# Optimization experiments

Hardware: AMD Instinct MI355X
Metric: run time of the kernel (lower is better)

The kernel has to match this reference:

```python
import jax, jax.numpy as jnp
import numpy as np
import math

B, SQ, SK, D = 16, 2048, 2048, 64


def setup_inputs() -> dict:
    key = jax.random.key(0)
    kq, kk, kv, kl = jax.random.split(key, 4)
    queries = jax.random.normal(kq, (B, SQ, D), dtype=jnp.float32)
    keys = jax.random.normal(kk, (B, SK, D), dtype=jnp.float32)
    values = jax.random.normal(kv, (B, SK, D), dtype=jnp.float32)
    # valid key lengths in [1, SK]
    valid_lens = jax.random.randint(kl, (B,), 1, SK + 1, dtype=jnp.int32)
    return {"queries": queries, "keys": keys, "values": values, "valid_lens": valid_lens}


def reference(queries, keys, values, valid_lens):
    d = queries.shape[-1]
    # [B, SQ, SK] raw scores
    scores = jnp.einsum("bqd,bkd->bqk", queries, keys) / math.sqrt(d)
    # masked_softmax: key positions >= valid_len are set to -1e6 (d2l semantics)
    kpos = jnp.arange(scores.shape[-1], dtype=jnp.int32)  # [SK]
    mask = kpos[None, None, :] < valid_lens[:, None, None]  # [B,1,SK] -> broadcast
    scores = jnp.where(mask, scores, jnp.float32(-1e6))
    attn = jax.nn.softmax(scores, axis=-1)
    # dropout rate is 0.0 -> identity
    return jnp.einsum("bqk,bkd->bqd", attn, values)
```

## Files before the change

### kernel.cpp

```cpp
#include <hip/hip_runtime.h>

#define NB 16
#define SQL 2048
#define SKL 2048
#define DH 64

typedef __attribute__((ext_vector_type(8)))  short bf16x8;
typedef __attribute__((ext_vector_type(4)))  unsigned short u16x4;
typedef __attribute__((ext_vector_type(8)))  unsigned short u16x8;
typedef __attribute__((ext_vector_type(4)))  float f32x4;
typedef __attribute__((ext_vector_type(16))) float f32x16;
typedef __attribute__((ext_vector_type(2)))  unsigned int u32x2;
typedef __attribute__((ext_vector_type(4)))  unsigned int u32x4;

#define SCL 0.18033688011112042f

__device__ __forceinline__ unsigned short f2bf(float f) {
    unsigned int u = __builtin_bit_cast(unsigned int, f);
    u += 0x7fffu + ((u >> 16) & 1u);
    return (unsigned short)(u >> 16);
}
__device__ __forceinline__ float bf2f(unsigned short h) {
    return __builtin_bit_cast(float, (unsigned int)h << 16);
}

__device__ __forceinline__ float fast_exp2(float x) {
#if __has_builtin(__builtin_amdgcn_exp2f)
    return __builtin_amdgcn_exp2f(x);
#else
    return exp2f(x);
#endif
}

__device__ __forceinline__ unsigned int cvt_pk_bf16(float a, float b) {
    unsigned int r;
    asm("v_cvt_pk_bf16_f32 %0, %1, %2" : "=v"(r) : "v"(a), "v"(b));
    return r;
}

__device__ __forceinline__ void lane32_swap(unsigned int &x, unsigned int &y) {
#if __has_builtin(__builtin_amdgcn_permlane32_swap)
    u32x2 r = __builtin_amdgcn_permlane32_swap(x, y, false, false);
    x = r[0]; y = r[1];
#else
    asm volatile("s_nop 1\n\tv_permlane32_swap_b32 %0, %1\n\ts_nop 1"
                 : "+v"(x), "+v"(y));
#endif
}

__global__ __launch_bounds__(256) void prep_kernel(
    const float* __restrict__ V, unsigned short* __restrict__ Vt) {
    const int blk = blockIdx.x;
    const int b   = blk >> 5;
    const int kb  = (blk & 31) << 6;
    __shared__ float tile[64][65];
    const int tid = threadIdx.x;
    {
        const int r  = tid >> 2;
        const int cg = (tid & 3) << 4;
        const float* vsrc = V + ((size_t)b * SKL + (kb + r)) * DH;
        #pragma unroll
        for (int i = 0; i < 4; ++i) {
            float4 x = *(const float4*)(vsrc + cg + i * 4);
            tile[r][cg + i*4 + 0] = x.x;
            tile[r][cg + i*4 + 1] = x.y;
            tile[r][cg + i*4 + 2] = x.z;
            tile[r][cg + i*4 + 3] = x.w;
        }
    }
    __syncthreads();
    {
        const int d  = tid >> 2;
        const int kg = (tid & 3) << 4;
        unsigned short* dst = Vt + ((size_t)b * DH + d) * SKL + kb + kg;
        u16x8 o0, o1;
        #pragma unroll
        for (int j = 0; j < 8; ++j) o0[j] = f2bf(tile[kg + j][d]);
        #pragma unroll
        for (int j = 0; j < 8; ++j) o1[j] = f2bf(tile[kg + 8 + j][d]);
        *(u16x8*)(dst)     = o0;
        *(u16x8*)(dst + 8) = o1;
    }
}

__global__ __launch_bounds__(256, 2) void attn_kernel(
    const float* __restrict__ Qf,
    const float* __restrict__ Kf,
    const unsigned short* __restrict__ Vt,
    const int* __restrict__ valid_lens,
    float* __restrict__ out) {
    const int b    = blockIdx.x;
    const int qblk = blockIdx.y;

    const int valid  = valid_lens[b];
    const int ntiles = (valid + 63) >> 6;

    const int tid  = threadIdx.x;
    const int lane = tid & 63;
    const int l31  = lane & 31;
    const int h2   = lane >> 5;
    const int sw   = l31 & 7;

    __shared__ unsigned short Klds[2][64][64];
    __shared__ unsigned short Vlds[2][64][64];

    const int q0 = qblk * 128 + (tid >> 6) * 32;
    const float* qptr = Qf + ((size_t)b * SQL + q0 + l31) * DH + h2 * 8;
    bf16x8 qf[4];
    #pragma unroll
    for (int ks = 0; ks < 4; ++ks) {
        float4 a0 = *(const float4*)(qptr + ks * 16);
        float4 a1 = *(const float4*)(qptr + ks * 16 + 4);
        u32x4 w = { cvt_pk_bf16(a0.x * SCL, a0.y * SCL),
                    cvt_pk_bf16(a0.z * SCL, a0.w * SCL),
                    cvt_pk_bf16(a1.x * SCL, a1.y * SCL),
                    cvt_pk_bf16(a1.z * SCL, a1.w * SCL) };
        qf[ks] = __builtin_bit_cast(bf16x8, w);
    }

    const float* kbase = Kf + (size_t)b * SKL * DH;
    const unsigned short* vbase = Vt + (size_t)b * DH * SKL;

    f32x16 o[2];
    #pragma unroll
    for (int i = 0; i < 2; ++i)
        #pragma unroll
        for (int r = 0; r < 16; ++r) o[i][r] = 0.f;
    float lr[4] = {0.f, 0.f, 0.f, 0.f};

    float4 kreg[2][2];
    u16x8  vreg[2];
    auto load_tile = [&](int kb0) {
        #pragma unroll
        for (int i = 0; i < 2; ++i) {
            const int c = i * 256 + tid, r = c >> 3, col = (c & 7) << 3;
            const float* kp = kbase + (size_t)(kb0 + r) * DH + col;
            kreg[i][0] = *(const float4*)(kp);
            kreg[i][1] = *(const float4*)(kp + 4);
            vreg[i]    = *(const u16x8*)(vbase + (size_t)r * SKL + kb0 + col);
        }
    };
    auto store_tile = [&](int buf) {
        #pragma unroll
        for (int i = 0; i < 2; ++i) {
            const int c = i * 256 + tid, r = c >> 3;
            const int pc = ((c & 7) ^ (r & 7)) << 3;
            u32x4 w = { cvt_pk_bf16(kreg[i][0].x, kreg[i][0].y),
                        cvt_pk_bf16(kreg[i][0].z, kreg[i][0].w),
                        cvt_pk_bf16(kreg[i][1].x, kreg[i][1].y),
                        cvt_pk_bf16(kreg[i][1].z, kreg[i][1].w) };
            *(u16x8*)&Klds[buf][r][pc] = __builtin_bit_cast(u16x8, w);
            *(u16x8*)&Vlds[buf][r][pc] = vreg[i];
        }
    };

    load_tile(0);
    store_tile(0);
    if (ntiles > 1) load_tile(64);
    __syncthreads();

    for (int kt = 0; kt < ntiles; ++kt) {
        const int kb  = kt << 6;
        const int cur = kt & 1;

        if (kt + 1 < ntiles) {
            store_tile(cur ^ 1);
            if (kt + 2 < ntiles) load_tile(kb + 128);
        }

        f32x16 s[2];
        #pragma unroll
        for (int t = 0; t < 2; ++t)
            #pragma unroll
            for (int r = 0; r < 16; ++r) s[t][r] = 0.f;
        __builtin_amdgcn_s_setprio(1);
        #pragma unroll
        for (int t = 0; t < 2; ++t)
            #pragma unroll
            for (int ks = 0; ks < 4; ++ks) {
                const bf16x8 kf = *(const bf16x8*)
                    &Klds[cur][t * 32 + l31][((2 * ks + h2) ^ sw) << 3];
                s[t] = __builtin_amdgcn_mfma_f32_32x32x16_bf16(kf, qf[ks], s[t], 0, 0, 0);
            }
        __builtin_amdgcn_s_setprio(0);

        if (kb + 64 > valid) {
            #pragma unroll
            for (int t = 0; t < 2; ++t)
                #pragma unroll
                for (int r = 0; r < 16; ++r)
                    if (kb + t * 32 + (r & 3) + 8 * (r >> 2) + 4 * h2 >= valid)
                        s[t][r] = -1e30f;
        }

        #pragma unroll
        for (int t = 0; t < 2; ++t)
            #pragma unroll
            for (int r = 0; r < 16; ++r) {
                const float p = fast_exp2(s[t][r]);
                s[t][r] = p;
                lr[r & 3] += p;
            }

        bf16x8 pf[4];
        #pragma unroll
        for (int t = 0; t < 2; ++t) {
            unsigned int w[4][2];
            #pragma unroll
            for (int a = 0; a < 4; ++a) {
                w[a][0] = cvt_pk_bf16(s[t][4 * a + 0], s[t][4 * a + 1]);
                w[a][1] = cvt_pk_bf16(s[t][4 * a + 2], s[t][4 * a + 3]);
            }
            #pragma unroll
            for (int i = 0; i < 2; ++i) {
                lane32_swap(w[0][i], w[1][i]);
                lane32_swap(w[2][i], w[3][i]);
            }
            u32x4 lo4 = { w[0][0], w[0][1], w[1][0], w[1][1] };
            u32x4 hi4 = { w[2][0], w[2][1], w[3][0], w[3][1] };
            pf[2 * t + 0] = __builtin_bit_cast(bf16x8, lo4);
            pf[2 * t + 1] = __builtin_bit_cast(bf16x8, hi4);
        }

        __builtin_amdgcn_s_setprio(1);
        #pragma unroll
        for (int dt = 0; dt < 2; ++dt)
            #pragma unroll
            for (int ks = 0; ks < 4; ++ks) {
                const bf16x8 vf = *(const bf16x8*)
                    &Vlds[cur][dt * 32 + l31][((2 * ks + h2) ^ sw) << 3];
                o[dt] = __builtin_amdgcn_mfma_f32_32x32x16_bf16(vf, pf[ks], o[dt], 0, 0, 0);
            }
        __builtin_amdgcn_s_setprio(0);

        __syncthreads();
    }

    float lrow = (lr[0] + lr[1]) + (lr[2] + lr[3]);
    lrow += __shfl_xor(lrow, 32);
    const float inv = 1.0f / lrow;

    float* op = out + ((size_t)b * SQL + q0 + l31) * DH;
    #pragma unroll
    for (int dt = 0; dt < 2; ++dt)
        #pragma unroll
        for (int g = 0; g < 4; ++g) {
            f32x4 ow;
            ow[0] = o[dt][g * 4 + 0] * inv; ow[1] = o[dt][g * 4 + 1] * inv;
            ow[2] = o[dt][g * 4 + 2] * inv; ow[3] = o[dt][g * 4 + 3] * inv;
            *(f32x4*)(op + dt * 32 + 8 * g + 4 * h2) = ow;
        }
}

extern "C" void kernel_launch(void* const* d_in, const int* in_sizes, int n_in,
                              void* d_out, int out_size, void* d_ws, size_t ws_size,
                              hipStream_t stream) {
    const float* Q  = (const float*)d_in[0];
    const float* K  = (const float*)d_in[1];
    const float* V  = (const float*)d_in[2];
    const int*   vl = (const int*)d_in[3];
    float* out = (float*)d_out;

    unsigned short* Vt = (unsigned short*)d_ws;

    prep_kernel<<<dim3(512), dim3(256), 0, stream>>>(V, Vt);
    attn_kernel<<<dim3(NB, SQL / 128), dim3(256), 0, stream>>>(
        Q, K, Vt, vl, out);
}
```

Baseline: 102.5 us.

## Split key tiles across wave pairs and merge partial outputs via LDS

Each block now handles 64 queries instead of 128, with 4 waves forming two pairs that process alternating key tiles (a split-K within the block). Partial outputs and row sums from the second pair are reduced through shared memory before the final normalization. This doubles the grid size and halves per-block serial key-loop length, improving parallelism and load balance across batches with varying valid lengths. The cost is doubled K/V global loads per query, more LDS (two tiles per stage), and an extra reduction and sync at the end.

```diff
diff --git a/kernel.cpp b/kernel.cpp
--- a/kernel.cpp
+++ b/kernel.cpp
@@ -19,9 +19,6 @@
     unsigned int u = __builtin_bit_cast(unsigned int, f);
     u += 0x7fffu + ((u >> 16) & 1u);
     return (unsigned short)(u >> 16);
-}
-__device__ __forceinline__ float bf2f(unsigned short h) {
-    return __builtin_bit_cast(float, (unsigned int)h << 16);
 }
 
 __device__ __forceinline__ float fast_exp2(float x) {
@@ -94,17 +91,21 @@
 
     const int valid  = valid_lens[b];
     const int ntiles = (valid + 63) >> 6;
+    const int rounds = (ntiles + 1) >> 1;
 
     const int tid  = threadIdx.x;
+    const int wave = tid >> 6;
+    const int pr   = wave >> 1;
+    const int qg   = wave & 1;
     const int lane = tid & 63;
     const int l31  = lane & 31;
     const int h2   = lane >> 5;
     const int sw   = l31 & 7;
 
-    __shared__ unsigned short Klds[2][64][64];
-    __shared__ unsigned short Vlds[2][64][64];
-
-    const int q0 = qblk * 128 + (tid >> 6) * 32;
+    __shared__ unsigned short Klds[2][2][64][64];
+    __shared__ unsigned short Vlds[2][2][64][64];
+
+    const int q0 = qblk * 64 + qg * 32;
     const float* qptr = Qf + ((size_t)b * SQL + q0 + l31) * DH + h2 * 8;
     bf16x8 qf[4];
     #pragma unroll
@@ -128,128 +129,166 @@
         for (int r = 0; r < 16; ++r) o[i][r] = 0.f;
     float lr[4] = {0.f, 0.f, 0.f, 0.f};
 
-    float4 kreg[2][2];
-    u16x8  vreg[2];
-    auto load_tile = [&](int kb0) {
-        #pragma unroll
-        for (int i = 0; i < 2; ++i) {
-            const int c = i * 256 + tid, r = c >> 3, col = (c & 7) << 3;
-            const float* kp = kbase + (size_t)(kb0 + r) * DH + col;
-            kreg[i][0] = *(const float4*)(kp);
-            kreg[i][1] = *(const float4*)(kp + 4);
-            vreg[i]    = *(const u16x8*)(vbase + (size_t)r * SKL + kb0 + col);
+    float4 kreg[2][2][2];
+    u16x8  vreg[2][2];
+    auto load_round = [&](int R) {
+        #pragma unroll
+        for (int p = 0; p < 2; ++p) {
+            const int ti = 2 * R + p;
+            if (ti < ntiles) {
+                const int kb0 = ti << 6;
+                #pragma unroll
+                for (int i = 0; i < 2; ++i) {
+                    const int c = i * 256 + tid, r = c >> 3, col = (c & 7) << 3;
+                    const float* kp = kbase + (size_t)(kb0 + r) * DH + col;
+                    kreg[p][i][0] = *(const float4*)(kp);
+                    kreg[p][i][1] = *(const float4*)(kp + 4);
+                    vreg[p][i]    = *(const u16x8*)(vbase + (size_t)r * SKL + kb0 + col);
+                }
+            }
         }
     };
-    auto store_tile = [&](int buf) {
-        #pragma unroll
-        for (int i = 0; i < 2; ++i) {
-            const int c = i * 256 + tid, r = c >> 3;
-            const int pc = ((c & 7) ^ (r & 7)) << 3;
-            u32x4 w = { cvt_pk_bf16(kreg[i][0].x, kreg[i][0].y),
-                        cvt_pk_bf16(kreg[i][0].z, kreg[i][0].w),
-                        cvt_pk_bf16(kreg[i][1].x, kreg[i][1].y),
-                        cvt_pk_bf16(kreg[i][1].z, kreg[i][1].w) };
-            *(u16x8*)&Klds[buf][r][pc] = __builtin_bit_cast(u16x8, w);
-            *(u16x8*)&Vlds[buf][r][pc] = vreg[i];
+    auto store_round = [&](int set, int R) {
+        #pragma unroll
+        for (int p = 0; p < 2; ++p) {
+            const int ti = 2 * R + p;
+            if (ti < ntiles) {
+                #pragma unroll
+                for (int i = 0; i < 2; ++i) {
+                    const int c = i * 256 + tid, r = c >> 3;
+                    const int pc = ((c & 7) ^ (r & 7)) << 3;
+                    u32x4 w = { cvt_pk_bf16(kreg[p][i][0].x, kreg[p][i][0].y),
+                                cvt_pk_bf16(kreg[p][i][0].z, kreg[p][i][0].w),
+                                cvt_pk_bf16(kreg[p][i][1].x, kreg[p][i][1].y),
+                                cvt_pk_bf16(kreg[p][i][1].z, kreg[p][i][1].w) };
+                    *(u16x8*)&Klds[set][p][r][pc] = __builtin_bit_cast(u16x8, w);
+                    *(u16x8*)&Vlds[set][p][r][pc] = vreg[p][i];
+                }
+            }
         }
     };
 
-    load_tile(0);
-    store_tile(0);
-    if (ntiles > 1) load_tile(64);
+    load_round(0);
+    store_round(0, 0);
+    if (rounds > 1) load_round(1);
     __syncthreads();
 
-    for (int kt = 0; kt < ntiles; ++kt) {
-        const int kb  = kt << 6;
-        const int cur = kt & 1;
-
-        if (kt + 1 < ntiles) {
-            store_tile(cur ^ 1);
-            if (kt + 2 < ntiles) load_tile(kb + 128);
-        }
-
-        f32x16 s[2];
-        #pragma unroll
-        for (int t = 0; t < 2; ++t)
-            #pragma unroll
-            for (int r = 0; r < 16; ++r) s[t][r] = 0.f;
-        __builtin_amdgcn_s_setprio(1);
-        #pragma unroll
-        for (int t = 0; t < 2; ++t)
-            #pragma unroll
-            for (int ks = 0; ks < 4; ++ks) {
-                const bf16x8 kf = *(const bf16x8*)
-                    &Klds[cur][t * 32 + l31][((2 * ks + h2) ^ sw) << 3];
-                s[t] = __builtin_amdgcn_mfma_f32_32x32x16_bf16(kf, qf[ks], s[t], 0, 0, 0);
-            }
-        __builtin_amdgcn_s_setprio(0);
-
-        if (kb + 64 > valid) {
+    for (int r = 0; r < rounds; ++r) {
+        const int rp = r & 1;
+        if (r + 1 < rounds) {
+            store_round(rp ^ 1, r + 1);
+            if (r + 2 < rounds) load_round(r + 2);
+        }
+
+        const int ti = 2 * r + pr;
+        if (ti < ntiles) {
+            const int kb = ti << 6;
+
+            f32x16 s[2];
             #pragma unroll
             for (int t = 0; t < 2; ++t)
                 #pragma unroll
-                for (int r = 0; r < 16; ++r)
-                    if (kb + t * 32 + (r & 3) + 8 * (r >> 2) + 4 * h2 >= valid)
-                        s[t][r] = -1e30f;
-        }
-
-        #pragma unroll
-        for (int t = 0; t < 2; ++t)
-            #pragma unroll
-            for (int r = 0; r < 16; ++r) {
-                const float p = fast_exp2(s[t][r]);
-                s[t][r] = p;
-                lr[r & 3] += p;
-            }
-
-        bf16x8 pf[4];
-        #pragma unroll
-        for (int t = 0; t < 2; ++t) {
-            unsigned int w[4][2];
-            #pragma unroll
-            for (int a = 0; a < 4; ++a) {
-                w[a][0] = cvt_pk_bf16(s[t][4 * a + 0], s[t][4 * a + 1]);
-                w[a][1] = cvt_pk_bf16(s[t][4 * a + 2], s[t][4 * a + 3]);
-            }
-            #pragma unroll
-            for (int i = 0; i < 2; ++i) {
-                lane32_swap(w[0][i], w[1][i]);
-                lane32_swap(w[2][i], w[3][i]);
-            }
-            u32x4 lo4 = { w[0][0], w[0][1], w[1][0], w[1][1] };
-            u32x4 hi4 = { w[2][0], w[2][1], w[3][0], w[3][1] };
-            pf[2 * t + 0] = __builtin_bit_cast(bf16x8, lo4);
-            pf[2 * t + 1] = __builtin_bit_cast(bf16x8, hi4);
-        }
-
-        __builtin_amdgcn_s_setprio(1);
+                for (int r2 = 0; r2 < 16; ++r2) s[t][r2] = 0.f;
+            __builtin_amdgcn_s_setprio(1);
+            #pragma unroll
+            for (int t = 0; t < 2; ++t)
+                #pragma unroll
+                for (int ks = 0; ks < 4; ++ks) {
+                    const bf16x8 kf = *(const bf16x8*)
+                        &Klds[rp][pr][t * 32 + l31][((2 * ks + h2) ^ sw) << 3];
+                    s[t] = __builtin_amdgcn_mfma_f32_32x32x16_bf16(kf, qf[ks], s[t], 0, 0, 0);
+                }
+            __builtin_amdgcn_s_setprio(0);
+
+            if (kb + 64 > valid) {
+                #pragma unroll
+                for (int t = 0; t < 2; ++t)
+                    #pragma unroll
+                    for (int r2 = 0; r2 < 16; ++r2)
+                        if (kb + t * 32 + (r2 & 3) + 8 * (r2 >> 2) + 4 * h2 >= valid)
+                            s[t][r2] = -1e30f;
+            }
+
+            #pragma unroll
+            for (int t = 0; t < 2; ++t)
+                #pragma unroll
+                for (int r2 = 0; r2 < 16; ++r2) {
+                    const float p = fast_exp2(s[t][r2]);
+                    s[t][r2] = p;
+                    lr[r2 & 3] += p;
+                }
+
+            bf16x8 pf[4];
+            #pragma unroll
+            for (int t = 0; t < 2; ++t) {
+                unsigned int w[4][2];
+                #pragma unroll
+                for (int a = 0; a < 4; ++a) {
+                    w[a][0] = cvt_pk_bf16(s[t][4 * a + 0], s[t][4 * a + 1]);
+                    w[a][1] = cvt_pk_bf16(s[t][4 * a + 2], s[t][4 * a + 3]);
+                }
+                #pragma unroll
+                for (int i = 0; i < 2; ++i) {
+                    lane32_swap(w[0][i], w[1][i]);
+                    lane32_swap(w[2][i], w[3][i]);
+                }
+                u32x4 lo4 = { w[0][0], w[0][1], w[1][0], w[1][1] };
+                u32x4 hi4 = { w[2][0], w[2][1], w[3][0], w[3][1] };
+                pf[2 * t + 0] = __builtin_bit_cast(bf16x8, lo4);
+                pf[2 * t + 1] = __builtin_bit_cast(bf16x8, hi4);
+            }
+
+            __builtin_amdgcn_s_setprio(1);
+            #pragma unroll
+            for (int dt = 0; dt < 2; ++dt)
+                #pragma unroll
+                for (int ks = 0; ks < 4; ++ks) {
+                    const bf16x8 vf = *(const bf16x8*)
+                        &Vlds[rp][pr][dt * 32 + l31][((2 * ks + h2) ^ sw) << 3];
+                    o[dt] = __builtin_amdgcn_mfma_f32_32x32x16_bf16(vf, pf[ks], o[dt], 0, 0, 0);
+                }
+            __builtin_amdgcn_s_setprio(0);
+        }
+
+        __syncthreads();
+    }
+
+    float lrow = (lr[0] + lr[1]) + (lr[2] + lr[3]);
+    float* obuf = (float*)&Klds[0][0][0][0];
+    float* lbuf = obuf + 2 * 32 * 68;
+    if (pr == 1) {
+        const int base = (qg * 32 + l31) * 68;
         #pragma unroll
         for (int dt = 0; dt < 2; ++dt)
             #pragma unroll
-            for (int ks = 0; ks < 4; ++ks) {
-                const bf16x8 vf = *(const bf16x8*)
-                    &Vlds[cur][dt * 32 + l31][((2 * ks + h2) ^ sw) << 3];
-                o[dt] = __builtin_amdgcn_mfma_f32_32x32x16_bf16(vf, pf[ks], o[dt], 0, 0, 0);
-            }
-        __builtin_amdgcn_s_setprio(0);
-
-        __syncthreads();
-    }
-
-    float lrow = (lr[0] + lr[1]) + (lr[2] + lr[3]);
-    lrow += __shfl_xor(lrow, 32);
-    const float inv = 1.0f / lrow;
-
-    float* op = out + ((size_t)b * SQL + q0 + l31) * DH;
-    #pragma unroll
-    for (int dt = 0; dt < 2; ++dt)
-        #pragma unroll
-        for (int g = 0; g < 4; ++g) {
-            f32x4 ow;
-            ow[0] = o[dt][g * 4 + 0] * inv; ow[1] = o[dt][g * 4 + 1] * inv;
-            ow[2] = o[dt][g * 4 + 2] * inv; ow[3] = o[dt][g * 4 + 3] * inv;
-            *(f32x4*)(op + dt * 32 + 8 * g + 4 * h2) = ow;
-        }
+            for (int g = 0; g < 4; ++g) {
+                f32x4 ow;
+                ow[0] = o[dt][g * 4 + 0]; ow[1] = o[dt][g * 4 + 1];
+                ow[2] = o[dt][g * 4 + 2]; ow[3] = o[dt][g * 4 + 3];
+                *(f32x4*)&obuf[base + dt * 32 + 8 * g + 4 * h2] = ow;
+            }
+        lbuf[(qg * 32 + l31) * 2 + h2] = lrow;
+    }
+    __syncthreads();
+    if (pr == 0) {
+        const int base = (qg * 32 + l31) * 68;
+        lrow += lbuf[(qg * 32 + l31) * 2 + h2];
+        lrow += __shfl_xor(lrow, 32);
+        const float inv = 1.0f / lrow;
+        float* op = out + ((size_t)b * SQL + q0 + l31) * DH;
+        #pragma unroll
+        for (int dt = 0; dt < 2; ++dt)
+            #pragma unroll
+            for (int g = 0; g < 4; ++g) {
+                const f32x4 pv = *(const f32x4*)&obuf[base + dt * 32 + 8 * g + 4 * h2];
+                f32x4 ow;
+                ow[0] = (o[dt][g * 4 + 0] + pv[0]) * inv;
+                ow[1] = (o[dt][g * 4 + 1] + pv[1]) * inv;
+                ow[2] = (o[dt][g * 4 + 2] + pv[2]) * inv;
+                ow[3] = (o[dt][g * 4 + 3] + pv[3]) * inv;
+                *(f32x4*)(op + dt * 32 + 8 * g + 4 * h2) = ow;
+            }
+    }
 }
 
 extern "C" void kernel_launch(void* const* d_in, const int* in_sizes, int n_in,
@@ -264,6 +303,6 @@
     unsigned short* Vt = (unsigned short*)d_ws;
 
     prep_kernel<<<dim3(512), dim3(256), 0, stream>>>(V, Vt);
-    attn_kernel<<<dim3(NB, SQL / 128), dim3(256), 0, stream>>>(
+    attn_kernel<<<dim3(NB, SQL / 64), dim3(256), 0, stream>>>(
         Q, K, Vt, vl, out);
 }
```

Result: no change. 103.3 us (+0.8%).
